# Optimization experiments

Measured on AMD Instinct MI355X. Metric: run time of the kernel, lower is better.

Reference implementation:

```python
import jax, jax.numpy as jnp
import numpy as np

EMBED_DIM = 1024
B, L = 4, 2048

def setup_inputs() -> dict:
    key = jax.random.key(0)
    ks = jax.random.split(key, 7)
    d = EMBED_DIM
    s = 1.0 / np.sqrt(d)
    return {
        "x": jax.random.normal(ks[0], (B, L, d), dtype=jnp.float32),
        "Wq": jax.random.uniform(ks[1], (d, d), jnp.float32, -s, s),
        "bq": jax.random.uniform(ks[2], (d,), jnp.float32, -s, s),
        "Wk": jax.random.uniform(ks[3], (d, d), jnp.float32, -s, s),
        "bk": jax.random.uniform(ks[4], (d,), jnp.float32, -s, s),
        "Wv": jax.random.uniform(ks[5], (d, d), jnp.float32, -s, s),
        "bv": jax.random.uniform(ks[6], (d,), jnp.float32, -s, s),
    }

def reference(x, Wq, bq, Wk, bk, Wv, bv):
    Bsz, Lq, d = x.shape
    # torch Linear: x @ W.T + b
    Q = jnp.einsum("bld,ed->ble", x, Wq) + bq
    K = jnp.einsum("bld,ed->ble", x, Wk) + bk
    V = jnp.einsum("bld,ed->ble", x, Wv) + bv
    # additive causal mask: strict upper triangle gets -999 (NOT -inf), per source
    mask = jnp.triu(jnp.ones((Lq, Lq), dtype=x.dtype), k=1) * (-999.0)
    scores = jnp.einsum("bqd,bkd->bqk", Q, K) / jnp.asarray(d, x.dtype) ** 0.5 + mask
    wts = jax.nn.softmax(scores, axis=2)
    out = jnp.einsum("bqk,bkd->bqd", wts, V)
    return (out, wts)
```

## Files before the change

### kernel.cpp

```cpp
#include <hip/hip_runtime.h>
#include <hip/hip_bf16.h>
#include <stdint.h>

#define BATCH 4
#define L_SEQ 2048
#define DIM   1024

typedef __bf16 bf16;
typedef __bf16 bf16x4 __attribute__((ext_vector_type(4)));
typedef __bf16 bf16x8 __attribute__((ext_vector_type(8)));
typedef float  f32x4  __attribute__((ext_vector_type(4)));

#define GLDS(src, dst) __builtin_amdgcn_global_load_lds(\
    (const __attribute__((address_space(1))) void*)(src), \
    (__attribute__((address_space(3))) void*)(dst), 16, 0, 0)

#define BARX() do { asm volatile("" ::: "memory"); \
                    __builtin_amdgcn_s_barrier(); \
                    asm volatile("" ::: "memory"); } while (0)

#define MFMA16 __builtin_amdgcn_mfma_f32_16x16x32_bf16

__global__ __launch_bounds__(256)
void cvt_all(const float* __restrict__ x,  const float* __restrict__ Wq,
             const float* __restrict__ Wk, const float* __restrict__ Wv,
             bf16* __restrict__ Xb, bf16* __restrict__ Wcat)
{
    const int b = blockIdx.x;
    const float* src; bf16* dst; int i;
    if (b < 8192) { src = x; dst = Xb; i = b * 256 + threadIdx.x; }
    else {
        int s = (b - 8192) >> 10;
        src = s == 0 ? Wq : (s == 1 ? Wk : Wv);
        dst = Wcat + (size_t)s * 1048576;
        i = ((b - 8192) & 1023) * 256 + threadIdx.x;
    }
    float4 v = ((const float4*)src)[i];
    bf16x4 o = { (bf16)v.x, (bf16)v.y, (bf16)v.z, (bf16)v.w };
    ((bf16x4*)dst)[i] = o;
}

template<int MODE, int BM, int BN, int NTH, int WM, int WN>
__global__ __launch_bounds__(NTH, 2)
void gemmX(const bf16* __restrict__ Abase, const bf16* __restrict__ Bbase,
           const float* __restrict__ bqp, const float* __restrict__ bkp,
           const float* __restrict__ bvp,
           void* __restrict__ o0, void* __restrict__ o1, void* __restrict__ o2)
{
    constexpr int MI  = BM / WM / 16;
    constexpr int ASZ = BM * 128;
    constexpr int BSZ = BN * 128;
    constexpr int PST = ASZ + BSZ;
    constexpr int SA  = ASZ / (NTH * 16);
    constexpr int SB  = BSZ / (NTH * 16);
    constexpr int SAB = SA + SB;
    static_assert(BN / WN / 16 == 4, "NJ must be 4");

    __shared__ __align__(16) char smem[2 * PST];

    int m0, n0, nt, z = blockIdx.z;
    const bf16 *Aop, *Bop;
    int lda, ldb;

    if constexpr (MODE == 0) {
        const int id = blockIdx.x;
        const int xcd = id & 7, i = id >> 3;
        const int mi = (xcd & 1) * 6 + i % 6;
        const int ni = (xcd >> 1) * 8 + i / 6;
        m0 = mi * 256; n0 = ni * 256; nt = 16;
        Aop = Abase; Bop = Bbase; lda = DIM; ldb = DIM;
    } else if constexpr (MODE == 2) {
        const int u = blockIdx.x;
        if (u >= 72) {
            int v = u - 72, qi = 0;
            while (v >= 14 - 2 * qi) { v -= 14 - 2 * qi; ++qi; }
            const int ki = 2 * qi + 2 + v;
            float* sc = (float*)o0 + (size_t)z * L_SEQ * L_SEQ;
            const int row = qi * 256 + (threadIdx.x >> 1);
            float* p = sc + (size_t)row * L_SEQ + ki * 128 + (threadIdx.x & 1) * 64;
            f32x4 z4 = {0.f, 0.f, 0.f, 0.f};
#pragma unroll
            for (int c = 0; c < 16; ++c) *(f32x4*)(p + c * 4) = z4;
            return;
        }
        int qi = 0;
        while ((qi + 1) * (qi + 2) <= u) ++qi;
        const int ki = u - qi * (qi + 1);
        m0 = ki * 128; n0 = qi * 256; nt = 16;
        Aop = Abase + (size_t)z * L_SEQ * DIM;
        Bop = Bbase + (size_t)z * L_SEQ * DIM;
        lda = DIM; ldb = DIM;
    } else {
        const int id = blockIdx.x;
        const int qi = 15 - (id >> 5);
        const int ei = (id >> 2) & 7;
        z = id & 3;
        m0 = ei * 128; n0 = qi * 128; nt = 2 * qi + 2;
        Aop = Abase + (size_t)z * DIM * L_SEQ;
        Bop = Bbase + (size_t)z * L_SEQ * L_SEQ;
        lda = L_SEQ; ldb = L_SEQ;
    }

    const int tid  = threadIdx.x;
    const int w    = tid >> 6, lane = tid & 63;
    const int wm   = w / WN, wn = w % WN;
    const int l15  = lane & 15, lh = lane >> 4;
    const int lr4  = lh << 2;

    auto stageA = [&](int t, int s) {
        const int p = s * (NTH * 16) + tid * 16;
        const int L = p ^ (((p >> 7) & 7) << 4);
        GLDS(Aop + (size_t)(m0 + (p >> 7)) * lda + ((t << 6) + ((L & 127) >> 1)),
             smem + (t & 1) * PST + (p - (lane << 4)));
    };
    auto stageB = [&](int t, int s) {
        const int p = s * (NTH * 16) + tid * 16;
        const int L = p ^ (((p >> 7) & 7) << 4);
        GLDS(Bop + (size_t)(n0 + (p >> 7)) * ldb + ((t << 6) + ((L & 127) >> 1)),
             smem + (t & 1) * PST + ASZ + (p - (lane << 4)));
    };

    const int swz = (l15 & 7) << 4;
    const int ko0 = (lh << 4) ^ swz;
    const int ko1 = (64 + (lh << 4)) ^ swz;
    const int arb = (wm * (BM / 2)) * 128;
    const int brb = ASZ + (wn * 64) * 128;

    f32x4 acc[MI][4];
#pragma unroll
    for (int i = 0; i < MI; ++i)
#pragma unroll
        for (int j = 0; j < 4; ++j) acc[i][j] = (f32x4){0.f, 0.f, 0.f, 0.f};

#define VMW() do { if constexpr (SAB == 8) asm volatile("s_waitcnt vmcnt(8)" ::: "memory"); \
                   else asm volatile("s_waitcnt vmcnt(6)" ::: "memory"); } while (0)

#pragma unroll
    for (int s = 0; s < SA; ++s) stageA(0, s);
#pragma unroll
    for (int s = 0; s < SB; ++s) stageB(0, s);
#pragma unroll
    for (int s = 0; s < SA; ++s) stageA(1, s);
#pragma unroll
    for (int s = 0; s < SB; ++s) stageB(1, s);
    VMW();
    BARX();

    auto ktile = [&](int t) {
        const bool pref = (t + 2 < nt);
        char* base = smem + (t & 1) * PST;
        bf16x8 af[MI / 2][2], bfr[4][2];

#pragma unroll
        for (int i = 0; i < MI / 2; ++i) {
            int ro = arb + (i * 16 + l15) * 128;
            af[i][0] = *(const bf16x8*)(base + ro + ko0);
            af[i][1] = *(const bf16x8*)(base + ro + ko1);
        }
#pragma unroll
        for (int j = 0; j < 2; ++j) {
            int ro = brb + (j * 16 + l15) * 128;
            bfr[j][0] = *(const bf16x8*)(base + ro + ko0);
            bfr[j][1] = *(const bf16x8*)(base + ro + ko1);
        }
        BARX();
        __builtin_amdgcn_s_setprio(1);
#pragma unroll
        for (int i = 0; i < MI / 2; ++i)
#pragma unroll
            for (int j = 0; j < 2; ++j) {
                acc[i][j] = MFMA16(af[i][0], bfr[j][0], acc[i][j], 0, 0, 0);
                acc[i][j] = MFMA16(af[i][1], bfr[j][1], acc[i][j], 0, 0, 0);
            }
        __builtin_amdgcn_s_setprio(0);
        BARX();

#pragma unroll
        for (int j = 0; j < 2; ++j) {
            int ro = brb + ((j + 2) * 16 + l15) * 128;
            bfr[j + 2][0] = *(const bf16x8*)(base + ro + ko0);
            bfr[j + 2][1] = *(const bf16x8*)(base + ro + ko1);
        }
        BARX();
        __builtin_amdgcn_s_setprio(1);
#pragma unroll
        for (int i = 0; i < MI / 2; ++i)
#pragma unroll
            for (int j = 0; j < 2; ++j) {
                acc[i][j + 2] = MFMA16(af[i][0], bfr[j + 2][0], acc[i][j + 2], 0, 0, 0);
                acc[i][j + 2] = MFMA16(af[i][1], bfr[j + 2][1], acc[i][j + 2], 0, 0, 0);
            }
        __builtin_amdgcn_s_setprio(0);
        BARX();

#pragma unroll
        for (int i = 0; i < MI / 2; ++i) {
            int ro = arb + ((MI / 2 + i) * 16 + l15) * 128;
            af[i][0] = *(const bf16x8*)(base + ro + ko0);
            af[i][1] = *(const bf16x8*)(base + ro + ko1);
        }
        if (pref) {
#pragma unroll
            for (int s = 0; s < SB; ++s) stageB(t + 2, s);
        }
        BARX();
        __builtin_amdgcn_s_setprio(1);
#pragma unroll
        for (int i = 0; i < MI / 2; ++i)
#pragma unroll
            for (int j = 0; j < 2; ++j) {
                acc[MI / 2 + i][j + 2] = MFMA16(af[i][0], bfr[j + 2][0], acc[MI / 2 + i][j + 2], 0, 0, 0);
                acc[MI / 2 + i][j + 2] = MFMA16(af[i][1], bfr[j + 2][1], acc[MI / 2 + i][j + 2], 0, 0, 0);
            }
        __builtin_amdgcn_s_setprio(0);
        BARX();

        if (pref) {
#pragma unroll
            for (int s = 0; s < SA; ++s) stageA(t + 2, s);
        }
        BARX();
        __builtin_amdgcn_s_setprio(1);
#pragma unroll
        for (int i = 0; i < MI / 2; ++i)
#pragma unroll
            for (int j = 0; j < 2; ++j) {
                acc[MI / 2 + i][j] = MFMA16(af[i][0], bfr[j][0], acc[MI / 2 + i][j], 0, 0, 0);
                acc[MI / 2 + i][j] = MFMA16(af[i][1], bfr[j][1], acc[MI / 2 + i][j], 0, 0, 0);
            }
        __builtin_amdgcn_s_setprio(0);
        if (pref)      VMW();
        else if (t + 1 < nt) asm volatile("s_waitcnt vmcnt(0)" ::: "memory");
        BARX();
    };

    for (int t = 0; t < nt; t += 2) { ktile(t); ktile(t + 1); }

    if constexpr (MODE == 0) {
        const int sel = m0 >> 10;
        const int eb  = (m0 & 1023) + wm * (BM / 2);
        if (sel < 2) {
            bf16* out = sel == 0 ? (bf16*)o0 : (bf16*)o1;
            const float* bias = sel == 0 ? bqp : bkp;
#pragma unroll
            for (int i = 0; i < MI; ++i) {
                int e0 = eb + i * 16 + lr4;
                float4 bb = *(const float4*)(bias + e0);
#pragma unroll
                for (int j = 0; j < 4; ++j) {
                    int l = n0 + wn * 64 + j * 16 + l15;
                    bf16x4 v = { (bf16)(acc[i][j][0] + bb.x), (bf16)(acc[i][j][1] + bb.y),
                                 (bf16)(acc[i][j][2] + bb.z), (bf16)(acc[i][j][3] + bb.w) };
                    *(bf16x4*)((bf16*)out + (size_t)l * DIM + e0) = v;
                }
            }
        } else {
            bf16* Vt = (bf16*)o2;
#pragma unroll
            for (int i = 0; i < MI; ++i) {
                int e0 = eb + i * 16 + lr4;
                float4 bb = *(const float4*)(bvp + e0);
                float bbr[4] = { bb.x, bb.y, bb.z, bb.w };
#pragma unroll
                for (int j = 0; j < 4; ++j) {
                    int lg = n0 + wn * 64 + j * 16 + l15;
                    int b = lg >> 11, l = lg & 2047;
#pragma unroll
                    for (int r = 0; r < 4; ++r)
                        Vt[((size_t)b * DIM + e0 + r) * L_SEQ + l] = (bf16)(acc[i][j][r] + bbr[r]);
                }
            }
        }
    } else if constexpr (MODE == 2) {
        float* sc = (float*)o0 + (size_t)z * L_SEQ * L_SEQ;
#pragma unroll
        for (int i = 0; i < MI; ++i) {
            int k0e = m0 + wm * (BM / 2) + i * 16 + lr4;
#pragma unroll
            for (int j = 0; j < 4; ++j) {
                int q = n0 + wn * 64 + j * 16 + l15;
                f32x4 v = acc[i][j] * 0.03125f;
                *(f32x4*)(sc + (size_t)q * L_SEQ + k0e) = v;
            }
        }
    } else {
        float* o = (float*)o0 + (size_t)z * L_SEQ * DIM;
#pragma unroll
        for (int i = 0; i < MI; ++i) {
            int e0 = m0 + wm * (BM / 2) + i * 16 + lr4;
#pragma unroll
            for (int j = 0; j < 4; ++j) {
                int q = n0 + wn * 64 + j * 16 + l15;
                *(f32x4*)(o + (size_t)q * DIM + e0) = acc[i][j];
            }
        }
    }
#undef VMW
}

__global__ __launch_bounds__(256)
void softmax_rows(float* __restrict__ wts, bf16* __restrict__ Pb)
{
    const int row = blockIdx.x;
    const int q = row & 2047;
    float* s = wts + (size_t)row * L_SEQ;
    bf16*  p = Pb  + (size_t)row * L_SEQ;
    const int t = threadIdx.x;
    const int lane = t & 63, w = t >> 6;
    const int k0 = t * 8;

    float v[8];
    if (k0 + 7 <= q) {
        float4 a = *(const float4*)(s + k0);
        float4 b = *(const float4*)(s + k0 + 4);
        v[0]=a.x; v[1]=a.y; v[2]=a.z; v[3]=a.w;
        v[4]=b.x; v[5]=b.y; v[6]=b.z; v[7]=b.w;
    } else {
#pragma unroll
        for (int c = 0; c < 8; ++c) {
            int k = k0 + c;
            v[c] = (k <= q) ? s[k] : -3.0e38f;
        }
    }

    float mx = v[0];
#pragma unroll
    for (int c = 1; c < 8; ++c) mx = fmaxf(mx, v[c]);
#pragma unroll
    for (int off = 32; off; off >>= 1) mx = fmaxf(mx, __shfl_xor(mx, off));
    __shared__ float redm[4];
    if (lane == 0) redm[w] = mx;
    __syncthreads();
    mx = fmaxf(fmaxf(redm[0], redm[1]), fmaxf(redm[2], redm[3]));

    float sm = 0.f;
#pragma unroll
    for (int c = 0; c < 8; ++c) {
        float e = __expf(v[c] - mx);
        v[c] = e;
        sm += e;
    }
#pragma unroll
    for (int off = 32; off; off >>= 1) sm += __shfl_xor(sm, off);
    __shared__ float reds[4];
    if (lane == 0) reds[w] = sm;
    __syncthreads();
    sm = reds[0] + reds[1] + reds[2] + reds[3];
    const float inv = 1.f / sm;

    if (k0 <= (q | 255)) {
        float o[8];
#pragma unroll
        for (int c = 0; c < 8; ++c) o[c] = v[c] * inv;
        float4 s0 = { o[0], o[1], o[2], o[3] };
        float4 s1 = { o[4], o[5], o[6], o[7] };
        *(float4*)(s + k0)     = s0;
        *(float4*)(s + k0 + 4) = s1;
        bf16x8 pb = { (bf16)o[0], (bf16)o[1], (bf16)o[2], (bf16)o[3],
                      (bf16)o[4], (bf16)o[5], (bf16)o[6], (bf16)o[7] };
        *(bf16x8*)(p + k0) = pb;
    }
}

extern "C" void kernel_launch(void* const* d_in, const int* in_sizes, int n_in,
                              void* d_out, int out_size, void* d_ws, size_t ws_size,
                              hipStream_t stream)
{
    const float* x  = (const float*)d_in[0];
    const float* Wq = (const float*)d_in[1];
    const float* bq = (const float*)d_in[2];
    const float* Wk = (const float*)d_in[3];
    const float* bk = (const float*)d_in[4];
    const float* Wv = (const float*)d_in[5];
    const float* bv = (const float*)d_in[6];

    float* out = (float*)d_out;
    float* wts = out + (size_t)BATCH * L_SEQ * DIM;

    char* ws = (char*)d_ws;
    bf16* Xb   = (bf16*)(ws + 0);
    bf16* Wcat = (bf16*)(ws + (16u  << 20));
    bf16* Qb   = (bf16*)(ws + (22u  << 20));
    bf16* Kb   = (bf16*)(ws + (38u  << 20));
    bf16* Vt   = (bf16*)(ws + (54u  << 20));
    bf16* Pb   = (bf16*)(ws + (70u  << 20));

    cvt_all<<<dim3(11264), dim3(256), 0, stream>>>(x, Wq, Wk, Wv, Xb, Wcat);

    gemmX<0, 256, 256, 512, 2, 4><<<dim3(384, 1, 1), dim3(512), 0, stream>>>(
        Wcat, Xb, bq, bk, bv, Qb, Kb, Vt);
    gemmX<2, 128, 256, 512, 2, 4><<<dim3(128, 1, 4), dim3(512), 0, stream>>>(
        Kb, Qb, nullptr, nullptr, nullptr, wts, nullptr, nullptr);
    softmax_rows<<<dim3(8192), dim3(256), 0, stream>>>(wts, Pb);
    gemmX<3, 128, 128, 256, 2, 2><<<dim3(512, 1, 1), dim3(256), 0, stream>>>(
        Vt, Pb, nullptr, nullptr, nullptr, out, nullptr, nullptr);
}
```

Baseline: 178.8 us.

## Use uniform 128x128 tiles for all GEMMs with finer causal tiling and interleaved PV scheduling

```diff
diff --git a/kernel.cpp b/kernel.cpp
--- a/kernel.cpp
+++ b/kernel.cpp
@@ -40,61 +40,47 @@
     ((bf16x4*)dst)[i] = o;
 }
 
-template<int MODE, int BM, int BN, int NTH, int WM, int WN>
-__global__ __launch_bounds__(NTH, 2)
-void gemmX(const bf16* __restrict__ Abase, const bf16* __restrict__ Bbase,
+template<int MODE>
+__global__ __launch_bounds__(256, 2)
+void gemmQ(const bf16* __restrict__ Abase, const bf16* __restrict__ Bbase,
            const float* __restrict__ bqp, const float* __restrict__ bkp,
            const float* __restrict__ bvp,
            void* __restrict__ o0, void* __restrict__ o1, void* __restrict__ o2)
 {
-    constexpr int MI  = BM / WM / 16;
-    constexpr int ASZ = BM * 128;
-    constexpr int BSZ = BN * 128;
-    constexpr int PST = ASZ + BSZ;
-    constexpr int SA  = ASZ / (NTH * 16);
-    constexpr int SB  = BSZ / (NTH * 16);
-    constexpr int SAB = SA + SB;
-    static_assert(BN / WN / 16 == 4, "NJ must be 4");
-
-    __shared__ __align__(16) char smem[2 * PST];
+    constexpr int PST = 32768;
+    __shared__ __align__(16) char smem[65536];
 
     int m0, n0, nt, z = blockIdx.z;
     const bf16 *Aop, *Bop;
     int lda, ldb;
 
     if constexpr (MODE == 0) {
-        const int id = blockIdx.x;
-        const int xcd = id & 7, i = id >> 3;
-        const int mi = (xcd & 1) * 6 + i % 6;
-        const int ni = (xcd >> 1) * 8 + i / 6;
-        m0 = mi * 256; n0 = ni * 256; nt = 16;
+        const int id = blockIdx.x, xcd = id & 7, r = id >> 3;
+        const int mi = r >> 3;
+        const int ni = xcd * 8 + (r & 7);
+        m0 = mi * 128; n0 = ni * 128; nt = 16;
         Aop = Abase; Bop = Bbase; lda = DIM; ldb = DIM;
     } else if constexpr (MODE == 2) {
         const int u = blockIdx.x;
-        if (u >= 72) {
-            int v = u - 72, qi = 0;
-            while (v >= 14 - 2 * qi) { v -= 14 - 2 * qi; ++qi; }
-            const int ki = 2 * qi + 2 + v;
+        const int qi = u >> 4, ki = u & 15;
+        if (ki > qi) {
             float* sc = (float*)o0 + (size_t)z * L_SEQ * L_SEQ;
-            const int row = qi * 256 + (threadIdx.x >> 1);
+            const int row = qi * 128 + (threadIdx.x >> 1);
             float* p = sc + (size_t)row * L_SEQ + ki * 128 + (threadIdx.x & 1) * 64;
             f32x4 z4 = {0.f, 0.f, 0.f, 0.f};
 #pragma unroll
             for (int c = 0; c < 16; ++c) *(f32x4*)(p + c * 4) = z4;
             return;
         }
-        int qi = 0;
-        while ((qi + 1) * (qi + 2) <= u) ++qi;
-        const int ki = u - qi * (qi + 1);
-        m0 = ki * 128; n0 = qi * 256; nt = 16;
+        m0 = ki * 128; n0 = qi * 128; nt = 16;
         Aop = Abase + (size_t)z * L_SEQ * DIM;
         Bop = Bbase + (size_t)z * L_SEQ * DIM;
         lda = DIM; ldb = DIM;
     } else {
-        const int id = blockIdx.x;
-        const int qi = 15 - (id >> 5);
-        const int ei = (id >> 2) & 7;
-        z = id & 3;
+        const int id = blockIdx.x, k = id >> 1;
+        const int qi = (id & 1) ? (k >> 5) : 15 - (k >> 5);
+        const int rem = k & 31, ei = rem >> 2;
+        z = rem & 3;
         m0 = ei * 128; n0 = qi * 128; nt = 2 * qi + 2;
         Aop = Abase + (size_t)z * DIM * L_SEQ;
         Bop = Bbase + (size_t)z * L_SEQ * L_SEQ;
@@ -103,70 +89,67 @@
 
     const int tid  = threadIdx.x;
     const int w    = tid >> 6, lane = tid & 63;
-    const int wm   = w / WN, wn = w % WN;
+    const int wm   = w >> 1, wn = w & 1;
     const int l15  = lane & 15, lh = lane >> 4;
     const int lr4  = lh << 2;
 
-    auto stageA = [&](int t, int s) {
-        const int p = s * (NTH * 16) + tid * 16;
-        const int L = p ^ (((p >> 7) & 7) << 4);
-        GLDS(Aop + (size_t)(m0 + (p >> 7)) * lda + ((t << 6) + ((L & 127) >> 1)),
-             smem + (t & 1) * PST + (p - (lane << 4)));
+    auto stageA = [&](int t) {
+#pragma unroll
+        for (int s = 0; s < 4; ++s) {
+            const int p = s * 4096 + tid * 16;
+            const int L = p ^ (((p >> 7) & 7) << 4);
+            GLDS(Aop + (size_t)(m0 + (p >> 7)) * lda + ((t << 6) + ((L & 127) >> 1)),
+                 smem + (t & 1) * PST + (p - (lane << 4)));
+        }
     };
-    auto stageB = [&](int t, int s) {
-        const int p = s * (NTH * 16) + tid * 16;
-        const int L = p ^ (((p >> 7) & 7) << 4);
-        GLDS(Bop + (size_t)(n0 + (p >> 7)) * ldb + ((t << 6) + ((L & 127) >> 1)),
-             smem + (t & 1) * PST + ASZ + (p - (lane << 4)));
+    auto stageB = [&](int t) {
+#pragma unroll
+        for (int s = 0; s < 4; ++s) {
+            const int p = s * 4096 + tid * 16;
+            const int L = p ^ (((p >> 7) & 7) << 4);
+            GLDS(Bop + (size_t)(n0 + (p >> 7)) * ldb + ((t << 6) + ((L & 127) >> 1)),
+                 smem + (t & 1) * PST + 16384 + (p - (lane << 4)));
+        }
     };
 
     const int swz = (l15 & 7) << 4;
     const int ko0 = (lh << 4) ^ swz;
     const int ko1 = (64 + (lh << 4)) ^ swz;
-    const int arb = (wm * (BM / 2)) * 128;
-    const int brb = ASZ + (wn * 64) * 128;
-
-    f32x4 acc[MI][4];
-#pragma unroll
-    for (int i = 0; i < MI; ++i)
+    const int aro = (wm * 64 + l15) * 128;
+    const int bro = 16384 + (wn * 64 + l15) * 128;
+
+    f32x4 acc[4][4];
+#pragma unroll
+    for (int i = 0; i < 4; ++i)
 #pragma unroll
         for (int j = 0; j < 4; ++j) acc[i][j] = (f32x4){0.f, 0.f, 0.f, 0.f};
 
-#define VMW() do { if constexpr (SAB == 8) asm volatile("s_waitcnt vmcnt(8)" ::: "memory"); \
-                   else asm volatile("s_waitcnt vmcnt(6)" ::: "memory"); } while (0)
-
-#pragma unroll
-    for (int s = 0; s < SA; ++s) stageA(0, s);
-#pragma unroll
-    for (int s = 0; s < SB; ++s) stageB(0, s);
-#pragma unroll
-    for (int s = 0; s < SA; ++s) stageA(1, s);
-#pragma unroll
-    for (int s = 0; s < SB; ++s) stageB(1, s);
-    VMW();
-    BARX();
+    stageA(0); stageB(0); stageA(1); stageB(1);
+    asm volatile("s_waitcnt vmcnt(8)" ::: "memory");
+    __builtin_amdgcn_s_barrier();
+    asm volatile("" ::: "memory");
 
     auto ktile = [&](int t) {
         const bool pref = (t + 2 < nt);
         char* base = smem + (t & 1) * PST;
-        bf16x8 af[MI / 2][2], bfr[4][2];
-
-#pragma unroll
-        for (int i = 0; i < MI / 2; ++i) {
-            int ro = arb + (i * 16 + l15) * 128;
+        bf16x8 af[2][2], bfr[4][2];
+
+#pragma unroll
+        for (int i = 0; i < 2; ++i) {
+            int ro = aro + i * 2048;
             af[i][0] = *(const bf16x8*)(base + ro + ko0);
             af[i][1] = *(const bf16x8*)(base + ro + ko1);
         }
 #pragma unroll
         for (int j = 0; j < 2; ++j) {
-            int ro = brb + (j * 16 + l15) * 128;
+            int ro = bro + j * 2048;
             bfr[j][0] = *(const bf16x8*)(base + ro + ko0);
             bfr[j][1] = *(const bf16x8*)(base + ro + ko1);
         }
         BARX();
         __builtin_amdgcn_s_setprio(1);
 #pragma unroll
-        for (int i = 0; i < MI / 2; ++i)
+        for (int i = 0; i < 2; ++i)
 #pragma unroll
             for (int j = 0; j < 2; ++j) {
                 acc[i][j] = MFMA16(af[i][0], bfr[j][0], acc[i][j], 0, 0, 0);
@@ -177,14 +160,14 @@
 
 #pragma unroll
         for (int j = 0; j < 2; ++j) {
-            int ro = brb + ((j + 2) * 16 + l15) * 128;
+            int ro = bro + (j + 2) * 2048;
             bfr[j + 2][0] = *(const bf16x8*)(base + ro + ko0);
             bfr[j + 2][1] = *(const bf16x8*)(base + ro + ko1);
         }
         BARX();
         __builtin_amdgcn_s_setprio(1);
 #pragma unroll
-        for (int i = 0; i < MI / 2; ++i)
+        for (int i = 0; i < 2; ++i)
 #pragma unroll
             for (int j = 0; j < 2; ++j) {
                 acc[i][j + 2] = MFMA16(af[i][0], bfr[j + 2][0], acc[i][j + 2], 0, 0, 0);
@@ -194,42 +177,36 @@
         BARX();
 
 #pragma unroll
-        for (int i = 0; i < MI / 2; ++i) {
-            int ro = arb + ((MI / 2 + i) * 16 + l15) * 128;
+        for (int i = 0; i < 2; ++i) {
+            int ro = aro + (i + 2) * 2048;
             af[i][0] = *(const bf16x8*)(base + ro + ko0);
             af[i][1] = *(const bf16x8*)(base + ro + ko1);
         }
-        if (pref) {
-#pragma unroll
-            for (int s = 0; s < SB; ++s) stageB(t + 2, s);
-        }
+        if (pref) stageB(t + 2);
         BARX();
         __builtin_amdgcn_s_setprio(1);
 #pragma unroll
-        for (int i = 0; i < MI / 2; ++i)
+        for (int i = 0; i < 2; ++i)
 #pragma unroll
             for (int j = 0; j < 2; ++j) {
-                acc[MI / 2 + i][j + 2] = MFMA16(af[i][0], bfr[j + 2][0], acc[MI / 2 + i][j + 2], 0, 0, 0);
-                acc[MI / 2 + i][j + 2] = MFMA16(af[i][1], bfr[j + 2][1], acc[MI / 2 + i][j + 2], 0, 0, 0);
+                acc[i + 2][j + 2] = MFMA16(af[i][0], bfr[j + 2][0], acc[i + 2][j + 2], 0, 0, 0);
+                acc[i + 2][j + 2] = MFMA16(af[i][1], bfr[j + 2][1], acc[i + 2][j + 2], 0, 0, 0);
             }
         __builtin_amdgcn_s_setprio(0);
         BARX();
 
-        if (pref) {
-#pragma unroll
-            for (int s = 0; s < SA; ++s) stageA(t + 2, s);
-        }
+        if (pref) stageA(t + 2);
         BARX();
         __builtin_amdgcn_s_setprio(1);
 #pragma unroll
-        for (int i = 0; i < MI / 2; ++i)
+        for (int i = 0; i < 2; ++i)
 #pragma unroll
             for (int j = 0; j < 2; ++j) {
-                acc[MI / 2 + i][j] = MFMA16(af[i][0], bfr[j][0], acc[MI / 2 + i][j], 0, 0, 0);
-                acc[MI / 2 + i][j] = MFMA16(af[i][1], bfr[j][1], acc[MI / 2 + i][j], 0, 0, 0);
+                acc[i + 2][j] = MFMA16(af[i][0], bfr[j][0], acc[i + 2][j], 0, 0, 0);
+                acc[i + 2][j] = MFMA16(af[i][1], bfr[j][1], acc[i + 2][j], 0, 0, 0);
             }
         __builtin_amdgcn_s_setprio(0);
-        if (pref)      VMW();
+        if (pref)            asm volatile("s_waitcnt vmcnt(8)" ::: "memory");
         else if (t + 1 < nt) asm volatile("s_waitcnt vmcnt(0)" ::: "memory");
         BARX();
     };
@@ -238,12 +215,12 @@
 
     if constexpr (MODE == 0) {
         const int sel = m0 >> 10;
-        const int eb  = (m0 & 1023) + wm * (BM / 2);
+        const int eb  = (m0 & 1023) + wm * 64;
         if (sel < 2) {
             bf16* out = sel == 0 ? (bf16*)o0 : (bf16*)o1;
             const float* bias = sel == 0 ? bqp : bkp;
 #pragma unroll
-            for (int i = 0; i < MI; ++i) {
+            for (int i = 0; i < 4; ++i) {
                 int e0 = eb + i * 16 + lr4;
                 float4 bb = *(const float4*)(bias + e0);
 #pragma unroll
@@ -257,7 +234,7 @@
         } else {
             bf16* Vt = (bf16*)o2;
 #pragma unroll
-            for (int i = 0; i < MI; ++i) {
+            for (int i = 0; i < 4; ++i) {
                 int e0 = eb + i * 16 + lr4;
                 float4 bb = *(const float4*)(bvp + e0);
                 float bbr[4] = { bb.x, bb.y, bb.z, bb.w };
@@ -274,8 +251,8 @@
     } else if constexpr (MODE == 2) {
         float* sc = (float*)o0 + (size_t)z * L_SEQ * L_SEQ;
 #pragma unroll
-        for (int i = 0; i < MI; ++i) {
-            int k0e = m0 + wm * (BM / 2) + i * 16 + lr4;
+        for (int i = 0; i < 4; ++i) {
+            int k0e = m0 + wm * 64 + i * 16 + lr4;
 #pragma unroll
             for (int j = 0; j < 4; ++j) {
                 int q = n0 + wn * 64 + j * 16 + l15;
@@ -286,8 +263,8 @@
     } else {
         float* o = (float*)o0 + (size_t)z * L_SEQ * DIM;
 #pragma unroll
-        for (int i = 0; i < MI; ++i) {
-            int e0 = m0 + wm * (BM / 2) + i * 16 + lr4;
+        for (int i = 0; i < 4; ++i) {
+            int e0 = m0 + wm * 64 + i * 16 + lr4;
 #pragma unroll
             for (int j = 0; j < 4; ++j) {
                 int q = n0 + wn * 64 + j * 16 + l15;
@@ -295,7 +272,6 @@
             }
         }
     }
-#undef VMW
 }
 
 __global__ __launch_bounds__(256)
@@ -348,7 +324,7 @@
     sm = reds[0] + reds[1] + reds[2] + reds[3];
     const float inv = 1.f / sm;
 
-    if (k0 <= (q | 255)) {
+    if (k0 <= (q | 127)) {
         float o[8];
 #pragma unroll
         for (int c = 0; c < 8; ++c) o[c] = v[c] * inv;
@@ -387,11 +363,11 @@
 
     cvt_all<<<dim3(11264), dim3(256), 0, stream>>>(x, Wq, Wk, Wv, Xb, Wcat);
 
-    gemmX<0, 256, 256, 512, 2, 4><<<dim3(384, 1, 1), dim3(512), 0, stream>>>(
+    gemmQ<0><<<dim3(1536, 1, 1), dim3(256), 0, stream>>>(
         Wcat, Xb, bq, bk, bv, Qb, Kb, Vt);
-    gemmX<2, 128, 256, 512, 2, 4><<<dim3(128, 1, 4), dim3(512), 0, stream>>>(
+    gemmQ<2><<<dim3(256, 1, 4), dim3(256), 0, stream>>>(
         Kb, Qb, nullptr, nullptr, nullptr, wts, nullptr, nullptr);
     softmax_rows<<<dim3(8192), dim3(256), 0, stream>>>(wts, Pb);
-    gemmX<3, 128, 128, 256, 2, 2><<<dim3(512, 1, 1), dim3(256), 0, stream>>>(
+    gemmQ<3><<<dim3(512, 1, 1), dim3(256), 0, stream>>>(
         Vt, Pb, nullptr, nullptr, nullptr, out, nullptr, nullptr);
 }
```

Result: faster. 167.3 us (-6.4%).
